# Kernel tuning notes

Hardware: AMD Instinct MI355X
Metric: run time of the kernel (lower is better)

## Reference

```python
import jax, jax.numpy as jnp
import numpy as np


def setup_inputs() -> dict:
    key = jax.random.key(0)
    k1, k2 = jax.random.split(key)
    imgs = jax.random.normal(k1, (16, 64, 64, 64), dtype=jnp.float32)
    # matches np.random.normal(0, 0.01, (1, inCs, outCs, filtSize, filtSize, 2))
    filts = 0.01 * jax.random.normal(k2, (1, 64, 64, 3, 3, 2), dtype=jnp.float32)
    return {"imgs": imgs, "filts": filts}


def reference(imgs, filts):
    # imgs:  [B, inC, H, W] real
    # filts: [1, inC, outC, fs, fs, 2] (real/imag planes)
    B, inC, H, W = imgs.shape
    fs = filts.shape[3]
    # zero-pad image to S = H + fs - 1 (full linear-conv FFT size)
    imgs_p = jnp.pad(imgs, ((0, 0), (0, 0), (0, fs - 1), (0, fs - 1)))
    img_f = jnp.fft.fftn(imgs_p, axes=(-2, -1))  # [B, inC, S, S] complex64
    # complex filter, padded to same FFT size
    fc = (filts[0, ..., 0] + 1j * filts[0, ..., 1]).astype(jnp.complex64)  # [inC, outC, fs, fs]
    fc_p = jnp.pad(fc, ((0, 0), (0, 0), (0, H - 1), (0, W - 1)))
    filt_f = jnp.fft.fftn(fc_p, axes=(-2, -1))  # [inC, outC, S, S]
    # Karatsuba complex multiply + sum over inC == complex contraction over inC.
    # Fused as one einsum instead of materializing [B,inC,outC,S,S] intermediates.
    out_f = jnp.einsum('bihw,iohw->bohw', img_f, filt_f)  # [B, outC, S, S]
    out = jnp.fft.ifftn(out_f, axes=(-2, -1))
    # crop [1:-1, 1:-1] and take real part, as in the torch module
    return out[:, :, 1:-1, 1:-1].real.astype(imgs.dtype)
```

## Files before the change

kernel.cpp:

```cpp
#include <hip/hip_runtime.h>


typedef _Float16 f16x8 __attribute__((ext_vector_type(8)));
typedef float    f32x4 __attribute__((ext_vector_type(4)));

#define NB 16
#define NC 64
#define NH 64
#define NW 64
#define CHUNKS 528
#define SLAB_BYTES (CHUNKS * 16)
#define WF_HALFS (9 * 2 * 4 * 64 * 8)

__global__ __launch_bounds__(256) void prep_w(const float* __restrict__ filts,
                                              _Float16* __restrict__ wf) {
    const int f = blockIdx.x * 256 + threadIdx.x;
    if (f >= WF_HALFS) return;
    const int e  = f & 7;
    const int l  = (f >> 3) & 63;
    const int n  = (f >> 9) & 3;
    const int kc = (f >> 11) & 1;
    const int t  = f >> 12;
    const int i  = kc * 32 + (l >> 4) * 8 + e;
    const int o  = n * 16 + (l & 15);
    const int ky = t / 3, kx = t % 3;
    wf[f] = (_Float16)filts[(((i * 64 + o) * 3 + ky) * 3 + kx) * 2];
}

__global__ __launch_bounds__(512, 4) void conv_direct(const float* __restrict__ imgs,
                                                      const _Float16* __restrict__ wf,
                                                      float* __restrict__ out) {
    __shared__ uint4 ldsb[4 * SLAB_BYTES / 16];
    char* lds = reinterpret_cast<char*>(ldsb);
    const int bid = blockIdx.x;
    const int swz = ((bid & 7) << 6) | (bid >> 3);
    const int b   = swz >> 5;
    const int y0  = (swz & 31) << 1;
    const int tid = threadIdx.x;
    const int w   = tid >> 6;
    const int l   = tid & 63;
    const int h   = l >> 4;
    const int r   = l & 15;

    {
        const int sl   = w >> 1;
        const int half = w & 1;
        const int y    = y0 + sl - 1;
        const bool yv  = ((unsigned)y < (unsigned)NH);
        char* slab = lds + sl * SLAB_BYTES;

        if (half == 0 && l < 16) {
            const int ci  = l >> 1;
            const int xp2 = (l & 1) ? 65 : 0;
            const int c2  = xp2 * 8 + (ci ^ (xp2 & 7));
            f16x8 z;
            #pragma unroll
            for (int k = 0; k < 8; ++k) z[k] = (_Float16)0.f;
            *reinterpret_cast<f16x8*>(slab + c2 * 16) = z;
        }

        float f[32];
        if (yv) {
            const float* src = imgs + (((size_t)(b * NC + half * 32)) * NH + y) * NW + l;
            #pragma unroll
            for (int j = 0; j < 32; ++j)
                f[j] = src[(size_t)j * NH * NW];
        } else {
            #pragma unroll
            for (int j = 0; j < 32; ++j) f[j] = 0.f;
        }

        const int xp = l + 1;
        #pragma unroll
        for (int cj = 0; cj < 4; ++cj) {
            const int ci = half * 4 + cj;
            f16x8 v;
            #pragma unroll
            for (int k = 0; k < 8; ++k) v[k] = (_Float16)f[cj * 8 + k];
            const int chunk = xp * 8 + (ci ^ (xp & 7));
            *reinterpret_cast<f16x8*>(slab + chunk * 16) = v;
        }
    }
    __syncthreads();

    const int row = w >> 2;
    const int xh  = (w >> 1) & 1;
    const int oh  = w & 1;

    f32x4 acc[2][2];
    #pragma unroll
    for (int m = 0; m < 2; ++m)
        #pragma unroll
        for (int n = 0; n < 2; ++n)
            acc[m][n] = f32x4{0.f, 0.f, 0.f, 0.f};

    #pragma unroll
    for (int ky = 0; ky < 3; ++ky) {
        const char* slab = lds + (row + 2 - ky) * SLAB_BYTES;
        #pragma unroll
        for (int kx = 0; kx < 3; ++kx) {
            const _Float16* wft = wf + (size_t)(ky * 3 + kx) * (2 * 4 * 64 * 8);
            #pragma unroll
            for (int kc = 0; kc < 2; ++kc) {
                f16x8 a[2], bb[2];
                #pragma unroll
                for (int m = 0; m < 2; ++m) {
                    const int xp = xh * 32 + m * 16 + r + 2 - kx;
                    const int chunk = xp * 8 + (((kc << 2) + h) ^ (xp & 7));
                    a[m] = *reinterpret_cast<const f16x8*>(slab + chunk * 16);
                }
                #pragma unroll
                for (int n = 0; n < 2; ++n)
                    bb[n] = *reinterpret_cast<const f16x8*>(
                        wft + ((size_t)((kc << 2) + (oh * 2 + n)) * 64 + l) * 8);
                #pragma unroll
                for (int m = 0; m < 2; ++m)
                    #pragma unroll
                    for (int n = 0; n < 2; ++n)
                        acc[m][n] = __builtin_amdgcn_mfma_f32_16x16x32_f16(a[m], bb[n], acc[m][n], 0, 0, 0);
            }
        }
    }

    const int y = y0 + row;
    #pragma unroll
    for (int m = 0; m < 2; ++m) {
        const int x0 = xh * 32 + m * 16 + h * 4;
        #pragma unroll
        for (int n = 0; n < 2; ++n) {
            const int o = oh * 32 + n * 16 + r;
            *reinterpret_cast<f32x4*>(out + (((size_t)(b * 64 + o) * 64 + y) * 64) + x0) = acc[m][n];
        }
    }
}

extern "C" void kernel_launch(void* const* d_in, const int* in_sizes, int n_in,
                              void* d_out, int out_size, void* d_ws, size_t ws_size,
                              hipStream_t stream) {
    const float* imgs  = (const float*)d_in[0];
    const float* filts = (const float*)d_in[1];
    float* out = (float*)d_out;
    _Float16* wfb = (_Float16*)d_ws;

    hipLaunchKernelGGL(prep_w, dim3((WF_HALFS + 255) / 256), dim3(256), 0, stream, filts, wfb);
    hipLaunchKernelGGL(conv_direct, dim3(NB * 32), dim3(512), 0, stream, imgs, wfb, out);
}
```

Before: 21.10 us.

## Process four output rows per block with prefetched second slab pair

Each block now computes four output rows instead of two, keeping six input slabs in LDS so halo rows are shared and fewer input rows are reloaded. The two extra input rows are fetched into registers before the first MFMA pass and written to LDS afterwards, so their global load latency overlaps compute. The grid is halved to 256 blocks, and launch bounds drop to 2 blocks per CU. The trade is less parallelism and occupancy on a 256-CU part plus higher register use, in exchange for lower input traffic and hidden load latency.

```diff
diff --git a/kernel.cpp b/kernel.cpp
--- a/kernel.cpp
+++ b/kernel.cpp
@@ -27,15 +27,15 @@
     wf[f] = (_Float16)filts[(((i * 64 + o) * 3 + ky) * 3 + kx) * 2];
 }
 
-__global__ __launch_bounds__(512, 4) void conv_direct(const float* __restrict__ imgs,
-                                                      const _Float16* __restrict__ wf,
-                                                      float* __restrict__ out) {
-    __shared__ uint4 ldsb[4 * SLAB_BYTES / 16];
+__global__ __launch_bounds__(512, 2) void conv_pipe(const float* __restrict__ imgs,
+                                                    const _Float16* __restrict__ wf,
+                                                    float* __restrict__ out) {
+    __shared__ uint4 ldsb[6 * SLAB_BYTES / 16];
     char* lds = reinterpret_cast<char*>(ldsb);
     const int bid = blockIdx.x;
-    const int swz = ((bid & 7) << 6) | (bid >> 3);
-    const int b   = swz >> 5;
-    const int y0  = (swz & 31) << 1;
+    const int swz = ((bid & 7) << 5) | (bid >> 3);
+    const int b   = swz >> 4;
+    const int y0  = (swz & 15) << 2;
     const int tid = threadIdx.x;
     const int w   = tid >> 6;
     const int l   = tid & 63;
@@ -45,7 +45,7 @@
     {
         const int sl   = w >> 1;
         const int half = w & 1;
-        const int y    = y0 + sl - 1;
+        const int y    = y0 - 1 + sl;
         const bool yv  = ((unsigned)y < (unsigned)NH);
         char* slab = lds + sl * SLAB_BYTES;
 
@@ -63,13 +63,11 @@
         if (yv) {
             const float* src = imgs + (((size_t)(b * NC + half * 32)) * NH + y) * NW + l;
             #pragma unroll
-            for (int j = 0; j < 32; ++j)
-                f[j] = src[(size_t)j * NH * NW];
+            for (int j = 0; j < 32; ++j) f[j] = src[(size_t)j * NH * NW];
         } else {
             #pragma unroll
             for (int j = 0; j < 32; ++j) f[j] = 0.f;
         }
-
         const int xp = l + 1;
         #pragma unroll
         for (int cj = 0; cj < 4; ++cj) {
@@ -81,18 +79,33 @@
             *reinterpret_cast<f16x8*>(slab + chunk * 16) = v;
         }
     }
+
+    const int s2 = 4 + (w >> 2);
+    const int q  = w & 3;
+    float pf[16];
+    {
+        const int y2 = y0 - 1 + s2;
+        if ((unsigned)y2 < (unsigned)NH) {
+            const float* src = imgs + (((size_t)(b * NC + q * 16)) * NH + y2) * NW + l;
+            #pragma unroll
+            for (int j = 0; j < 16; ++j) pf[j] = src[(size_t)j * NH * NW];
+        } else {
+            #pragma unroll
+            for (int j = 0; j < 16; ++j) pf[j] = 0.f;
+        }
+    }
     __syncthreads();
 
     const int row = w >> 2;
     const int xh  = (w >> 1) & 1;
     const int oh  = w & 1;
-
-    f32x4 acc[2][2];
+    const int xbase = xh * 32 + r + 2;
+
+    f32x4 acc0[2][2];
     #pragma unroll
     for (int m = 0; m < 2; ++m)
         #pragma unroll
-        for (int n = 0; n < 2; ++n)
-            acc[m][n] = f32x4{0.f, 0.f, 0.f, 0.f};
+        for (int n = 0; n < 2; ++n) acc0[m][n] = f32x4{0.f, 0.f, 0.f, 0.f};
 
     #pragma unroll
     for (int ky = 0; ky < 3; ++ky) {
@@ -105,7 +118,7 @@
                 f16x8 a[2], bb[2];
                 #pragma unroll
                 for (int m = 0; m < 2; ++m) {
-                    const int xp = xh * 32 + m * 16 + r + 2 - kx;
+                    const int xp = xbase + m * 16 - kx;
                     const int chunk = xp * 8 + (((kc << 2) + h) ^ (xp & 7));
                     a[m] = *reinterpret_cast<const f16x8*>(slab + chunk * 16);
                 }
@@ -117,19 +130,92 @@
                 for (int m = 0; m < 2; ++m)
                     #pragma unroll
                     for (int n = 0; n < 2; ++n)
-                        acc[m][n] = __builtin_amdgcn_mfma_f32_16x16x32_f16(a[m], bb[n], acc[m][n], 0, 0, 0);
-            }
-        }
-    }
-
-    const int y = y0 + row;
-    #pragma unroll
-    for (int m = 0; m < 2; ++m) {
-        const int x0 = xh * 32 + m * 16 + h * 4;
-        #pragma unroll
-        for (int n = 0; n < 2; ++n) {
-            const int o = oh * 32 + n * 16 + r;
-            *reinterpret_cast<f32x4*>(out + (((size_t)(b * 64 + o) * 64 + y) * 64) + x0) = acc[m][n];
+                        acc0[m][n] = __builtin_amdgcn_mfma_f32_16x16x32_f16(a[m], bb[n], acc0[m][n], 0, 0, 0);
+            }
+        }
+    }
+
+    {
+        char* slab = lds + s2 * SLAB_BYTES;
+        if (q == 0 && l < 16) {
+            const int ci  = l >> 1;
+            const int xp2 = (l & 1) ? 65 : 0;
+            const int c2  = xp2 * 8 + (ci ^ (xp2 & 7));
+            f16x8 z;
+            #pragma unroll
+            for (int k = 0; k < 8; ++k) z[k] = (_Float16)0.f;
+            *reinterpret_cast<f16x8*>(slab + c2 * 16) = z;
+        }
+        const int xp = l + 1;
+        #pragma unroll
+        for (int cj = 0; cj < 2; ++cj) {
+            const int ci = q * 2 + cj;
+            f16x8 v;
+            #pragma unroll
+            for (int k = 0; k < 8; ++k) v[k] = (_Float16)pf[cj * 8 + k];
+            const int chunk = xp * 8 + (ci ^ (xp & 7));
+            *reinterpret_cast<f16x8*>(slab + chunk * 16) = v;
+        }
+    }
+    __syncthreads();
+
+    {
+        const int y = y0 + row;
+        #pragma unroll
+        for (int m = 0; m < 2; ++m) {
+            const int x0 = xh * 32 + m * 16 + h * 4;
+            #pragma unroll
+            for (int n = 0; n < 2; ++n) {
+                const int o = oh * 32 + n * 16 + r;
+                *reinterpret_cast<f32x4*>(out + (((size_t)(b * 64 + o) * 64 + y) * 64) + x0) = acc0[m][n];
+            }
+        }
+    }
+
+    f32x4 acc1[2][2];
+    #pragma unroll
+    for (int m = 0; m < 2; ++m)
+        #pragma unroll
+        for (int n = 0; n < 2; ++n) acc1[m][n] = f32x4{0.f, 0.f, 0.f, 0.f};
+
+    #pragma unroll
+    for (int ky = 0; ky < 3; ++ky) {
+        const char* slab = lds + (row + 4 - ky) * SLAB_BYTES;
+        #pragma unroll
+        for (int kx = 0; kx < 3; ++kx) {
+            const _Float16* wft = wf + (size_t)(ky * 3 + kx) * (2 * 4 * 64 * 8);
+            #pragma unroll
+            for (int kc = 0; kc < 2; ++kc) {
+                f16x8 a[2], bb[2];
+                #pragma unroll
+                for (int m = 0; m < 2; ++m) {
+                    const int xp = xbase + m * 16 - kx;
+                    const int chunk = xp * 8 + (((kc << 2) + h) ^ (xp & 7));
+                    a[m] = *reinterpret_cast<const f16x8*>(slab + chunk * 16);
+                }
+                #pragma unroll
+                for (int n = 0; n < 2; ++n)
+                    bb[n] = *reinterpret_cast<const f16x8*>(
+                        wft + ((size_t)((kc << 2) + (oh * 2 + n)) * 64 + l) * 8);
+                #pragma unroll
+                for (int m = 0; m < 2; ++m)
+                    #pragma unroll
+                    for (int n = 0; n < 2; ++n)
+                        acc1[m][n] = __builtin_amdgcn_mfma_f32_16x16x32_f16(a[m], bb[n], acc1[m][n], 0, 0, 0);
+            }
+        }
+    }
+
+    {
+        const int y = y0 + 2 + row;
+        #pragma unroll
+        for (int m = 0; m < 2; ++m) {
+            const int x0 = xh * 32 + m * 16 + h * 4;
+            #pragma unroll
+            for (int n = 0; n < 2; ++n) {
+                const int o = oh * 32 + n * 16 + r;
+                *reinterpret_cast<f32x4*>(out + (((size_t)(b * 64 + o) * 64 + y) * 64) + x0) = acc1[m][n];
+            }
         }
     }
 }
@@ -143,5 +229,5 @@
     _Float16* wfb = (_Float16*)d_ws;
 
     hipLaunchKernelGGL(prep_w, dim3((WF_HALFS + 255) / 256), dim3(256), 0, stream, filts, wfb);
-    hipLaunchKernelGGL(conv_direct, dim3(NB * 32), dim3(512), 0, stream, imgs, wfb, out);
+    hipLaunchKernelGGL(conv_pipe, dim3(256), dim3(512), 0, stream, imgs, wfb, out);
 }
```

New measurement: 21.55 us. +2.1%, slower.
